# Optimization experiments

Hardware: AMD Instinct MI355X
Metric: run time of the kernel (lower is better)

Reference implementation:

```python
import jax, jax.numpy as jnp
import numpy as np

MODEL_BATCHES = 2048
NUM_POINTS = 8192
N_FUNCS = 8
REMOVE_ITERS = 51  # remove_points = 51 * model_batches -> first 51 iterations dropped


def setup_inputs() -> dict:
    key = jax.random.key(0)
    k1, k2, k3, k4, k5 = jax.random.split(key, 5)
    point = jax.random.normal(k1, (MODEL_BATCHES, 2, 1), dtype=jnp.float32) * 0.1
    optimized_weights = jax.random.normal(k2, (N_FUNCS, 2, 2), dtype=jnp.float32) * 0.5
    optimized_biases = jax.random.normal(k3, (N_FUNCS, 2, 1), dtype=jnp.float32) * 0.5
    optimized_function_ops = jax.random.uniform(k4, (N_FUNCS,), dtype=jnp.float32)
    index = jax.random.randint(k5, (MODEL_BATCHES, NUM_POINTS), 0, N_FUNCS, dtype=jnp.int32)
    return {
        "point": point,
        "optimized_weights": optimized_weights,
        "optimized_biases": optimized_biases,
        "optimized_function_ops": optimized_function_ops,
        "index": index,
    }


def reference(point, optimized_weights, optimized_biases, optimized_function_ops, index):
    mb = point.shape[0]

    def step(p, idx):  # p: [mb,2,1], idx: [mb]
        W = optimized_weights[idx]          # [mb,2,2]
        b = optimized_biases[idx]           # [mb,2,1]
        op = optimized_function_ops[idx]    # [mb]
        p_new = jnp.einsum('bij,bjk->bik', W, p) + b  # [mb,2,1]
        out = jnp.concatenate([p_new[:, :, 0], op[:, None]], axis=1)  # [mb,3]
        return p_new, out

    # scan over iterations: index.T is [num_points, mb]
    _, outs = jax.lax.scan(step, point, index.T)  # outs: [num_points, mb, 3]
    pts = outs.reshape(-1, 3)  # matches torch.cat along dim 0 then squeeze
    return pts[REMOVE_ITERS * mb:, :]
```

## Files before the change

kernel.cpp:

```cpp
#include <hip/hip_runtime.h>

#define MB   2048
#define NP   8192
#define NF   8
#define RM   51
#define NCH  64
#define CH   128

typedef float f32x4 __attribute__((ext_vector_type(4)));


__global__ __launch_bounds__(256) void ifs_phase1(
    const int* __restrict__ idxg, const float* __restrict__ W,
    const float* __restrict__ B, float4* __restrict__ maps)
{
    __shared__ int tile[256][33];
    __shared__ __align__(16) float tbl[NF][8];
    const int tid = threadIdx.x;
    if (tid < NF) {
        tbl[tid][0] = W[tid*4+0]; tbl[tid][1] = W[tid*4+1];
        tbl[tid][2] = W[tid*4+2]; tbl[tid][3] = W[tid*4+3];
        tbl[tid][4] = B[tid*2+0]; tbl[tid][5] = B[tid*2+1];
        tbl[tid][6] = 0.f;        tbl[tid][7] = 0.f;
    }
    const int c  = blockIdx.x >> 3;
    const int b0 = (blockIdx.x & 7) << 8;
    const int x4 = tid & 7, yy = tid >> 3;

    float a00 = 1.f, a01 = 0.f, a10 = 0.f, a11 = 1.f, c0 = 0.f, c1 = 0.f;

    for (int seg = 0; seg < 4; ++seg) {
        const int tb = c * CH + seg * 32;
        #pragma unroll
        for (int p = 0; p < 8; ++p) {
            const int row = yy + p * 32;
            const int4 v = *(const int4*)(idxg + (size_t)(b0 + row) * NP + tb + x4 * 4);
            tile[row][x4*4+0] = v.x; tile[row][x4*4+1] = v.y;
            tile[row][x4*4+2] = v.z; tile[row][x4*4+3] = v.w;
        }
        __syncthreads();
        #pragma unroll
        for (int s = 0; s < 32; ++s) {
            const int f = tile[tid][s];
            const float4 wl = *(const float4*)&tbl[f][0];
            const float4 wh = *(const float4*)&tbl[f][4];
            const float na00 = wl.x*a00 + wl.y*a10;
            const float na01 = wl.x*a01 + wl.y*a11;
            const float na10 = wl.z*a00 + wl.w*a10;
            const float na11 = wl.z*a01 + wl.w*a11;
            const float nc0  = wl.x*c0  + wl.y*c1 + wh.x;
            const float nc1  = wl.z*c0  + wl.w*c1 + wh.y;
            a00 = na00; a01 = na01; a10 = na10; a11 = na11; c0 = nc0; c1 = nc1;
        }
        __syncthreads();
    }
    const size_t n = ((size_t)c * MB + b0 + tid) * 2;
    maps[n]     = make_float4(a00, a01, a10, a11);
    maps[n + 1] = make_float4(c0,  c1,  0.f, 0.f);
}

__global__ __launch_bounds__(64) void ifs_phase2(
    const float2* __restrict__ point, const float4* __restrict__ maps,
    float2* __restrict__ pe)
{
    const int b = blockIdx.x * 64 + threadIdx.x;
    float2 p = point[b];
    float4 lo[8], hi[8], nlo[8], nhi[8];
    #pragma unroll
    for (int k = 0; k < 8; ++k) {
        lo[k] = maps[((size_t)k * MB + b) * 2];
        hi[k] = maps[((size_t)k * MB + b) * 2 + 1];
    }
    for (int g = 0; g < 8; ++g) {
        if (g < 7) {
            #pragma unroll
            for (int k = 0; k < 8; ++k) {
                nlo[k] = maps[((size_t)((g + 1) * 8 + k) * MB + b) * 2];
                nhi[k] = maps[((size_t)((g + 1) * 8 + k) * MB + b) * 2 + 1];
            }
        }
        #pragma unroll
        for (int k = 0; k < 8; ++k) {
            pe[(size_t)(g * 8 + k) * MB + b] = p;
            const float nx = lo[k].x * p.x + lo[k].y * p.y + hi[k].x;
            const float ny = lo[k].z * p.x + lo[k].w * p.y + hi[k].y;
            p.x = nx; p.y = ny;
        }
        #pragma unroll
        for (int k = 0; k < 8; ++k) { lo[k] = nlo[k]; hi[k] = nhi[k]; }
    }
}

template <bool CHECK>
__device__ __forceinline__ void phase3_body(
    const int* __restrict__ idxg, const float4* tA, const float4* tB,
    float (*sbuf)[4][256][3], int (*tile)[36],
    int c, int b0, int tid, const float2* __restrict__ pe,
    float* __restrict__ out)
{
    const int x4 = tid & 7, yy = tid >> 3;
    float2 p = pe[(size_t)c * MB + b0 + tid];

    int s_[3], r_[3];
    #pragma unroll
    for (int k = 0; k < 3; ++k) {
        const int w = 4 * (tid + 256 * k);
        s_[k] = w / 768;
        r_[k] = w - s_[k] * 768;
    }
    long long off[3];
    #pragma unroll
    for (int k = 0; k < 3; ++k)
        off[k] = (long long)(c * CH + s_[k] - RM) * (MB * 3) + b0 * 3 + r_[k];

    int gg = 0;
    for (int seg = 0; seg < 4; ++seg) {
        const int tb = c * CH + seg * 32;
        #pragma unroll
        for (int p8 = 0; p8 < 8; ++p8) {
            const int row = yy + p8 * 32;
            *(int4*)&tile[row][x4*4] = *(const int4*)(idxg + (size_t)(b0 + row) * NP + tb + x4 * 4);
        }
        __syncthreads();
        #pragma unroll
        for (int g = 0; g < 8; ++g, ++gg) {
            const int buf = gg & 1;
            const int4 f4 = *(const int4*)&tile[tid][g*4];
            const int fs[4] = {f4.x, f4.y, f4.z, f4.w};
            #pragma unroll
            for (int s = 0; s < 4; ++s) {
                const float4 w  = tA[fs[s]];
                const float4 bb = tB[fs[s]];
                const float nx = w.x * p.x + w.y * p.y + bb.x;
                const float ny = w.z * p.x + w.w * p.y + bb.y;
                p.x = nx; p.y = ny;
                sbuf[buf][s][tid][0] = p.x;
                sbuf[buf][s][tid][1] = p.y;
                sbuf[buf][s][tid][2] = bb.z;
            }
            __syncthreads();
            const int t0 = seg * 32 + g * 4;
            const float* flat = &sbuf[buf][0][0][0];
            #pragma unroll
            for (int k = 0; k < 3; ++k) {
                if (!CHECK || (t0 + s_[k]) >= RM) {
                    const f32x4 v = *(const f32x4*)(flat + 4 * (tid + 256 * k));
                    __builtin_nontemporal_store(v, (f32x4*)(out + off[k]));
                }
                off[k] += 4LL * (MB * 3);
            }
        }
        __syncthreads();
    }
}

template <bool DUMMY>
__global__ __launch_bounds__(256) void ifs_phase3(
    const int* __restrict__ idxg, const float* __restrict__ W,
    const float* __restrict__ B, const float* __restrict__ OPS,
    const float2* __restrict__ pe, float* __restrict__ out)
{
    __shared__ int tile[256][36];
    __shared__ __align__(16) float sbuf[2][4][256][3];
    __shared__ __align__(16) float4 tA[NF];
    __shared__ __align__(16) float4 tB[NF];
    const int tid = threadIdx.x;
    if (tid < NF) {
        tA[tid] = make_float4(W[tid*4+0], W[tid*4+1], W[tid*4+2], W[tid*4+3]);
        tB[tid] = make_float4(B[tid*2+0], B[tid*2+1], OPS[tid], 0.f);
    }

    const int c  = blockIdx.x >> 3;
    const int b0 = (blockIdx.x & 7) << 8;

    if (c == 0) phase3_body<true >(idxg, tA, tB, sbuf, tile, c, b0, tid, pe, out);
    else        phase3_body<false>(idxg, tA, tB, sbuf, tile, c, b0, tid, pe, out);
}

extern "C" void kernel_launch(void* const* d_in, const int* in_sizes, int n_in,
                              void* d_out, int out_size, void* d_ws, size_t ws_size,
                              hipStream_t stream) {
    const float* point = (const float*)d_in[0];
    const float* W     = (const float*)d_in[1];
    const float* B     = (const float*)d_in[2];
    const float* OPS   = (const float*)d_in[3];
    const int*   idx   = (const int*)  d_in[4];
    float*       out   = (float*)d_out;

    float*  ws   = (float*)d_ws;
    float4* maps = (float4*)ws;
    float2* pe   = (float2*)(ws + (size_t)NCH * MB * 8);

    ifs_phase1<<<NCH * (MB / 256), 256, 0, stream>>>(idx, W, B, maps);
    ifs_phase2<<<MB / 64, 64, 0, stream>>>((const float2*)point, maps, pe);
    ifs_phase3<false><<<NCH * (MB / 256), 256, 0, stream>>>(idx, W, B, OPS, pe, out);
}
```

Measured before the change: 70.78 us.

## Fuse three IFS phases into one persistent kernel with global atomic barriers

Merges the map-composition, prefix, and output phases into a single kernel of 512 blocks that synchronize through global atomic counters. The index tile is packed into bytes in shared memory and kept resident, so phase 3 reuses it instead of re-reading the index array from global memory, and staging of the next segment overlaps with compute. This removes two kernel launches and a second full read of the index data. In exchange it relies on all 512 blocks being co-resident to avoid deadlock, adds a memset launch, and serializes the prefix step on 8 blocks while the others spin.

Result: slower. 195.6 us (+176.4%).

```diff
diff --git a/kernel.cpp b/kernel.cpp
--- a/kernel.cpp
+++ b/kernel.cpp
@@ -7,100 +7,121 @@
 #define NCH  64
 #define CH   128
 
-typedef float f32x4 __attribute__((ext_vector_type(4)));
+typedef float        f32x4 __attribute__((ext_vector_type(4)));
+typedef unsigned int u32;
 
 
-__global__ __launch_bounds__(256) void ifs_phase1(
-    const int* __restrict__ idxg, const float* __restrict__ W,
-    const float* __restrict__ B, float4* __restrict__ maps)
+__global__ __launch_bounds__(256, 2) void ifs_fused(
+    const float2* __restrict__ point, const float* __restrict__ W,
+    const float* __restrict__ B, const float* __restrict__ OPS,
+    const int* __restrict__ idxg,
+    float4* __restrict__ mapsA, float2* __restrict__ mapsC,
+    float2* __restrict__ pe, int* __restrict__ bar,
+    float* __restrict__ out)
 {
-    __shared__ int tile[256][33];
-    __shared__ __align__(16) float tbl[NF][8];
+    __shared__ u32 ptile[256][35];
+    __shared__ __align__(16) float4 tA[NF];
+    __shared__ __align__(16) float4 tB[NF];
+    __shared__ __align__(16) float sbuf[4][256][3];
+
     const int tid = threadIdx.x;
+    const int bid = blockIdx.x;
+    const int c   = bid >> 3;
+    const int b0  = (bid & 7) << 8;
+    const int b   = b0 + tid;
+
     if (tid < NF) {
-        tbl[tid][0] = W[tid*4+0]; tbl[tid][1] = W[tid*4+1];
-        tbl[tid][2] = W[tid*4+2]; tbl[tid][3] = W[tid*4+3];
-        tbl[tid][4] = B[tid*2+0]; tbl[tid][5] = B[tid*2+1];
-        tbl[tid][6] = 0.f;        tbl[tid][7] = 0.f;
+        tA[tid] = make_float4(W[tid*4+0], W[tid*4+1], W[tid*4+2], W[tid*4+3]);
+        tB[tid] = make_float4(B[tid*2+0], B[tid*2+1], OPS[tid], 0.f);
     }
-    const int c  = blockIdx.x >> 3;
-    const int b0 = (blockIdx.x & 7) << 8;
-    const int x4 = tid & 7, yy = tid >> 3;
+    const int x8 = tid & 7, yy = tid >> 3;
 
-    float a00 = 1.f, a01 = 0.f, a10 = 0.f, a11 = 1.f, c0 = 0.f, c1 = 0.f;
-
-    for (int seg = 0; seg < 4; ++seg) {
-        const int tb = c * CH + seg * 32;
+    auto stage = [&](int seg) {
         #pragma unroll
         for (int p = 0; p < 8; ++p) {
             const int row = yy + p * 32;
-            const int4 v = *(const int4*)(idxg + (size_t)(b0 + row) * NP + tb + x4 * 4);
-            tile[row][x4*4+0] = v.x; tile[row][x4*4+1] = v.y;
-            tile[row][x4*4+2] = v.z; tile[row][x4*4+3] = v.w;
+            const int4 v = *(const int4*)(idxg + (size_t)(b0 + row) * NP
+                                          + c * CH + seg * 32 + x8 * 4);
+            ptile[row][seg * 8 + x8] =
+                (u32)v.x | ((u32)v.y << 8) | ((u32)v.z << 16) | ((u32)v.w << 24);
         }
-        __syncthreads();
+    };
+    stage(0);
+    __syncthreads();
+
+    float a00 = 1.f, a01 = 0.f, a10 = 0.f, a11 = 1.f, c0 = 0.f, c1 = 0.f;
+    for (int seg = 0; seg < 4; ++seg) {
+        if (seg < 3) stage(seg + 1);
         #pragma unroll
-        for (int s = 0; s < 32; ++s) {
-            const int f = tile[tid][s];
-            const float4 wl = *(const float4*)&tbl[f][0];
-            const float4 wh = *(const float4*)&tbl[f][4];
-            const float na00 = wl.x*a00 + wl.y*a10;
-            const float na01 = wl.x*a01 + wl.y*a11;
-            const float na10 = wl.z*a00 + wl.w*a10;
-            const float na11 = wl.z*a01 + wl.w*a11;
-            const float nc0  = wl.x*c0  + wl.y*c1 + wh.x;
-            const float nc1  = wl.z*c0  + wl.w*c1 + wh.y;
-            a00 = na00; a01 = na01; a10 = na10; a11 = na11; c0 = nc0; c1 = nc1;
+        for (int j = 0; j < 8; ++j) {
+            const u32 pc = ptile[tid][seg * 8 + j];
+            #pragma unroll
+            for (int e = 0; e < 4; ++e) {
+                const int f = (pc >> (8 * e)) & 7;
+                const float4 wl = tA[f];
+                const float4 wh = tB[f];
+                const float na00 = wl.x*a00 + wl.y*a10;
+                const float na01 = wl.x*a01 + wl.y*a11;
+                const float na10 = wl.z*a00 + wl.w*a10;
+                const float na11 = wl.z*a01 + wl.w*a11;
+                const float nc0  = wl.x*c0  + wl.y*c1 + wh.x;
+                const float nc1  = wl.z*c0  + wl.w*c1 + wh.y;
+                a00 = na00; a01 = na01; a10 = na10; a11 = na11; c0 = nc0; c1 = nc1;
+            }
         }
         __syncthreads();
     }
-    const size_t n = ((size_t)c * MB + b0 + tid) * 2;
-    maps[n]     = make_float4(a00, a01, a10, a11);
-    maps[n + 1] = make_float4(c0,  c1,  0.f, 0.f);
-}
+    mapsA[(size_t)c * MB + b] = make_float4(a00, a01, a10, a11);
+    mapsC[(size_t)c * MB + b] = make_float2(c0, c1);
 
-__global__ __launch_bounds__(64) void ifs_phase2(
-    const float2* __restrict__ point, const float4* __restrict__ maps,
-    float2* __restrict__ pe)
-{
-    const int b = blockIdx.x * 64 + threadIdx.x;
-    float2 p = point[b];
-    float4 lo[8], hi[8], nlo[8], nhi[8];
-    #pragma unroll
-    for (int k = 0; k < 8; ++k) {
-        lo[k] = maps[((size_t)k * MB + b) * 2];
-        hi[k] = maps[((size_t)k * MB + b) * 2 + 1];
-    }
-    for (int g = 0; g < 8; ++g) {
-        if (g < 7) {
+    __threadfence();
+    __syncthreads();
+    if (tid == 0)
+        __hip_atomic_fetch_add(&bar[0], 1, __ATOMIC_ACQ_REL, __HIP_MEMORY_SCOPE_AGENT);
+
+    if (c == 0) {
+        if (tid == 0)
+            while (__hip_atomic_load(&bar[0], __ATOMIC_ACQUIRE, __HIP_MEMORY_SCOPE_AGENT) < 512)
+                __builtin_amdgcn_s_sleep(2);
+        __syncthreads();
+
+        float2 p = point[b];
+        float4 A0[8]; float2 C0[8]; float4 A1[8]; float2 C1[8];
+        #pragma unroll
+        for (int k = 0; k < 8; ++k) {
+            A0[k] = mapsA[(size_t)k * MB + b];
+            C0[k] = mapsC[(size_t)k * MB + b];
+        }
+        for (int g = 0; g < 8; ++g) {
+            if (g < 7) {
+                #pragma unroll
+                for (int k = 0; k < 8; ++k) {
+                    A1[k] = mapsA[(size_t)((g + 1) * 8 + k) * MB + b];
+                    C1[k] = mapsC[(size_t)((g + 1) * 8 + k) * MB + b];
+                }
+            }
             #pragma unroll
             for (int k = 0; k < 8; ++k) {
-                nlo[k] = maps[((size_t)((g + 1) * 8 + k) * MB + b) * 2];
-                nhi[k] = maps[((size_t)((g + 1) * 8 + k) * MB + b) * 2 + 1];
+                pe[(size_t)(g * 8 + k) * MB + b] = p;
+                const float nx = A0[k].x * p.x + A0[k].y * p.y + C0[k].x;
+                const float ny = A0[k].z * p.x + A0[k].w * p.y + C0[k].y;
+                p.x = nx; p.y = ny;
             }
+            #pragma unroll
+            for (int k = 0; k < 8; ++k) { A0[k] = A1[k]; C0[k] = C1[k]; }
         }
-        #pragma unroll
-        for (int k = 0; k < 8; ++k) {
-            pe[(size_t)(g * 8 + k) * MB + b] = p;
-            const float nx = lo[k].x * p.x + lo[k].y * p.y + hi[k].x;
-            const float ny = lo[k].z * p.x + lo[k].w * p.y + hi[k].y;
-            p.x = nx; p.y = ny;
-        }
-        #pragma unroll
-        for (int k = 0; k < 8; ++k) { lo[k] = nlo[k]; hi[k] = nhi[k]; }
+        __threadfence();
+        __syncthreads();
+        if (tid == 0)
+            __hip_atomic_fetch_add(&bar[1], 1, __ATOMIC_ACQ_REL, __HIP_MEMORY_SCOPE_AGENT);
     }
-}
 
-template <bool CHECK>
-__device__ __forceinline__ void phase3_body(
-    const int* __restrict__ idxg, const float4* tA, const float4* tB,
-    float (*sbuf)[4][256][3], int (*tile)[36],
-    int c, int b0, int tid, const float2* __restrict__ pe,
-    float* __restrict__ out)
-{
-    const int x4 = tid & 7, yy = tid >> 3;
-    float2 p = pe[(size_t)c * MB + b0 + tid];
+    if (tid == 0)
+        while (__hip_atomic_load(&bar[1], __ATOMIC_ACQUIRE, __HIP_MEMORY_SCOPE_AGENT) < 8)
+            __builtin_amdgcn_s_sleep(2);
+    __syncthreads();
 
+    float2 p = pe[(size_t)c * MB + b];
     int s_[3], r_[3];
     #pragma unroll
     for (int k = 0; k < 3; ++k) {
@@ -113,68 +134,34 @@
     for (int k = 0; k < 3; ++k)
         off[k] = (long long)(c * CH + s_[k] - RM) * (MB * 3) + b0 * 3 + r_[k];
 
-    int gg = 0;
-    for (int seg = 0; seg < 4; ++seg) {
-        const int tb = c * CH + seg * 32;
+    const bool chk = (c == 0);
+    for (int grp = 0; grp < 32; ++grp) {
+        const u32 pc = ptile[tid][grp];
         #pragma unroll
-        for (int p8 = 0; p8 < 8; ++p8) {
-            const int row = yy + p8 * 32;
-            *(int4*)&tile[row][x4*4] = *(const int4*)(idxg + (size_t)(b0 + row) * NP + tb + x4 * 4);
+        for (int s = 0; s < 4; ++s) {
+            const int f = (pc >> (8 * s)) & 7;
+            const float4 wl = tA[f];
+            const float4 wh = tB[f];
+            const float nx = wl.x * p.x + wl.y * p.y + wh.x;
+            const float ny = wl.z * p.x + wl.w * p.y + wh.y;
+            p.x = nx; p.y = ny;
+            sbuf[s][tid][0] = p.x;
+            sbuf[s][tid][1] = p.y;
+            sbuf[s][tid][2] = wh.z;
         }
         __syncthreads();
+        const int t0 = grp * 4;
+        const float* flat = &sbuf[0][0][0];
         #pragma unroll
-        for (int g = 0; g < 8; ++g, ++gg) {
-            const int buf = gg & 1;
-            const int4 f4 = *(const int4*)&tile[tid][g*4];
-            const int fs[4] = {f4.x, f4.y, f4.z, f4.w};
-            #pragma unroll
-            for (int s = 0; s < 4; ++s) {
-                const float4 w  = tA[fs[s]];
-                const float4 bb = tB[fs[s]];
-                const float nx = w.x * p.x + w.y * p.y + bb.x;
-                const float ny = w.z * p.x + w.w * p.y + bb.y;
-                p.x = nx; p.y = ny;
-                sbuf[buf][s][tid][0] = p.x;
-                sbuf[buf][s][tid][1] = p.y;
-                sbuf[buf][s][tid][2] = bb.z;
+        for (int k = 0; k < 3; ++k) {
+            if (!chk || (t0 + s_[k]) >= RM) {
+                const f32x4 v = *(const f32x4*)(flat + 4 * (tid + 256 * k));
+                __builtin_nontemporal_store(v, (f32x4*)(out + off[k]));
             }
-            __syncthreads();
-            const int t0 = seg * 32 + g * 4;
-            const float* flat = &sbuf[buf][0][0][0];
-            #pragma unroll
-            for (int k = 0; k < 3; ++k) {
-                if (!CHECK || (t0 + s_[k]) >= RM) {
-                    const f32x4 v = *(const f32x4*)(flat + 4 * (tid + 256 * k));
-                    __builtin_nontemporal_store(v, (f32x4*)(out + off[k]));
-                }
-                off[k] += 4LL * (MB * 3);
-            }
+            off[k] += 4LL * (MB * 3);
         }
         __syncthreads();
     }
-}
-
-template <bool DUMMY>
-__global__ __launch_bounds__(256) void ifs_phase3(
-    const int* __restrict__ idxg, const float* __restrict__ W,
-    const float* __restrict__ B, const float* __restrict__ OPS,
-    const float2* __restrict__ pe, float* __restrict__ out)
-{
-    __shared__ int tile[256][36];
-    __shared__ __align__(16) float sbuf[2][4][256][3];
-    __shared__ __align__(16) float4 tA[NF];
-    __shared__ __align__(16) float4 tB[NF];
-    const int tid = threadIdx.x;
-    if (tid < NF) {
-        tA[tid] = make_float4(W[tid*4+0], W[tid*4+1], W[tid*4+2], W[tid*4+3]);
-        tB[tid] = make_float4(B[tid*2+0], B[tid*2+1], OPS[tid], 0.f);
-    }
-
-    const int c  = blockIdx.x >> 3;
-    const int b0 = (blockIdx.x & 7) << 8;
-
-    if (c == 0) phase3_body<true >(idxg, tA, tB, sbuf, tile, c, b0, tid, pe, out);
-    else        phase3_body<false>(idxg, tA, tB, sbuf, tile, c, b0, tid, pe, out);
 }
 
 extern "C" void kernel_launch(void* const* d_in, const int* in_sizes, int n_in,
@@ -187,11 +174,13 @@
     const int*   idx   = (const int*)  d_in[4];
     float*       out   = (float*)d_out;
 
-    float*  ws   = (float*)d_ws;
-    float4* maps = (float4*)ws;
-    float2* pe   = (float2*)(ws + (size_t)NCH * MB * 8);
+    char* ws = (char*)d_ws;
+    float4* mapsA = (float4*)(ws);
+    float2* mapsC = (float2*)(ws + (size_t)NCH * MB * 16);
+    float2* pe    = (float2*)(ws + (size_t)NCH * MB * 24);
+    int*    bar   = (int*)   (ws + (size_t)NCH * MB * 32);
 
-    ifs_phase1<<<NCH * (MB / 256), 256, 0, stream>>>(idx, W, B, maps);
-    ifs_phase2<<<MB / 64, 64, 0, stream>>>((const float2*)point, maps, pe);
-    ifs_phase3<false><<<NCH * (MB / 256), 256, 0, stream>>>(idx, W, B, OPS, pe, out);
+    hipMemsetAsync(bar, 0, 128, stream);
+    ifs_fused<<<NCH * (MB / 256), 256, 0, stream>>>(
+        (const float2*)point, W, B, OPS, idx, mapsA, mapsC, pe, bar, out);
 }
```
